# Kernel tuning notes

Measured on AMD Instinct MI355X. Metric: run time of the kernel, lower is better.

## Reference

```python
import jax, jax.numpy as jnp
import numpy as np

B, N, L, P = 128, 128, 64, 30  # batch, max_nodes, latent_dim, n_perms
LOG2PI = float(np.log(2.0 * np.pi))


def setup_inputs() -> dict:
    key = jax.random.key(0)
    k_mu, k_ls, k_eps, k_w, k_adj, k_mask, k_perm = jax.random.split(key, 7)
    mu = jax.random.normal(k_mu, (B, L), dtype=jnp.float32)
    logstd = 0.1 * jax.random.normal(k_ls, (B, L), dtype=jnp.float32)
    eps = jax.random.normal(k_eps, (B, L), dtype=jnp.float32)
    W_dec = 0.02 * jax.random.normal(k_w, (L, N * N), dtype=jnp.float32)
    Adj = jax.random.randint(k_adj, (B, N, N), 0, 2, dtype=jnp.int32)
    # symmetric adjacency, zero diagonal
    Adj = jnp.triu(Adj, 1)
    Adj = Adj + jnp.swapaxes(Adj, 1, 2)
    # per-graph node counts -> block masks marking valid node pairs
    n_nodes = jax.random.randint(k_mask, (B,), N // 2, N + 1)  # [B]
    valid = jnp.arange(N)[None, :] < n_nodes[:, None]          # [B, N]
    node_masks = (valid[:, :, None] & valid[:, None, :]).astype(jnp.int32)
    # true random permutations, one per (i, j) pair as in the torch loop
    perm_keys = jax.random.split(k_perm, B * P)
    perms = jax.vmap(lambda kk: jax.random.permutation(kk, N))(perm_keys)
    perms = perms.reshape(B, P, N).astype(jnp.int32)
    return {"mu": mu, "logstd": logstd, "eps": eps, "W_dec": W_dec,
            "Adj": Adj, "node_masks": node_masks, "perms": perms}


def _masked_perm_logprob(logit, A, m, perm):
    # logit: [N,N] Bernoulli logits; A, m: [N,N]; perm: [N]
    lp = logit[perm][:, perm]  # symmetric permutation of rows and cols
    logp = A * jax.nn.log_sigmoid(lp) + (1.0 - A) * jax.nn.log_sigmoid(-lp)
    return jnp.sum(logp * m)


def reference(mu, logstd, eps, W_dec, Adj, node_masks, perms):
    # q = Normal(mu, exp(logstd)); z = q.rsample()
    z = mu + eps * jnp.exp(logstd)                      # [B, L]
    logits = (z @ W_dec).reshape(B, N, N)               # decoder Bernoulli logits
    # Faithful to torch loop: rec_errors[i, j] uses logits[j], Adj[j], mask[j]
    # with an independent random permutation per (i, j).
    l_p = logits[:P]                                    # [P, N, N]
    A_p = Adj[:P].astype(logits.dtype)
    m_p = node_masks[:P].astype(logits.dtype)
    rec_errors = jax.vmap(
        lambda perm_i: jax.vmap(_masked_perm_logprob)(l_p, A_p, m_p, perm_i)
    )(perms)                                            # [B, P]
    RE = jnp.sum(jnp.max(rec_errors, axis=1))           # scalar
    # KL = log q(z) - log p(z), Independent Normal over latent dim
    log_q = jnp.sum(-0.5 * eps * eps - logstd - 0.5 * LOG2PI, axis=-1)  # [B]
    log_p = jnp.sum(-0.5 * z * z - 0.5 * LOG2PI, axis=-1)               # [B]
    KL = log_q - log_p
    elbo = jnp.mean(RE - KL)
    return -elbo
```

## Files before the change

kernel.cpp:

```cpp
#include <hip/hip_runtime.h>
#include <hip/hip_fp16.h>
#include <math.h>

#define Bn 128
#define Nn 128
#define Ln 64
#define Pn 30
#define PG 10

#define TOFF  0
#define BOFF  491520
#define VOFFW 506880
#define ROFF  510720
#define KLOFF 514560

__global__ __launch_bounds__(256) void k_prep(const float* __restrict__ mu,
                                              const float* __restrict__ logstd,
                                              const float* __restrict__ eps,
                                              const float* __restrict__ W,
                                              const int* __restrict__ Adj,
                                              const int* __restrict__ nm,
                                              float* __restrict__ ws) {
    int blk = blockIdx.x, t = threadIdx.x;
    if (blk < 192) {
        int chunk = blk & 63, pg = blk >> 6;
        __shared__ float zs[PG][Ln];
        for (int idx = t; idx < PG * Ln; idx += 256) {
            int g = pg * PG * Ln + idx;
            zs[idx / Ln][idx % Ln] = mu[g] + eps[g] * __expf(logstd[g]);
        }
        __syncthreads();
        int uv = chunk * 256 + t;
        float acc[PG];
#pragma unroll
        for (int q = 0; q < PG; q++) acc[q] = 0.f;
        for (int k = 0; k < Ln; k++) {
            float w = W[k * (Nn * Nn) + uv];
#pragma unroll
            for (int q = 0; q < PG; q++) acc[q] = fmaf(zs[q][k], w, acc[q]);
        }
        uint32_t* tab = (uint32_t*)ws;
#pragma unroll
        for (int q = 0; q < PG; q++) {
            int p = pg * PG + q;
            float l = acc[q];
            float nl = -l;
            float lsneg = (nl < 0.f) ? (nl - log1pf(__expf(nl))) : (-log1pf(__expf(-nl)));
            __half2 h = __floats2half2_rn(lsneg, l);
            tab[p * (Nn * Nn) + uv] = *(uint32_t*)&h;
        }
    } else if (blk < 192 + 4 * Pn) {
        int pb = blk - 192;
        int p  = pb >> 2;
        int qr = pb & 3;
        __shared__ float val_s[Nn];
        if (t < Nn) {
            float v = (float)nm[p * Nn * Nn + t * Nn + t];
            val_s[t] = v;
            ws[VOFFW + p * Nn + t] = v;
        }
        __syncthreads();
        int sub = t >> 6, lane = t & 63;
        int ioff = sub >> 1, ch = sub & 1;
        int j = ch * 64 + lane;
        uint32_t* Bp = (uint32_t*)ws + BOFF + p * Nn * 4;
        for (int ib = qr * 32; ib < qr * 32 + 32; ib += 2) {
            int i = ib + ioff;
            bool pred = (Adj[p * Nn * Nn + i * Nn + j] != 0) &&
                        (val_s[i] != 0.f) && (val_s[j] != 0.f);
            unsigned long long m = __ballot(pred);
            if (lane == 0) {
                Bp[i * 4 + ch * 2]     = (uint32_t)m;
                Bp[i * 4 + ch * 2 + 1] = (uint32_t)(m >> 32);
            }
        }
    } else {
        float kl = 0.f;
        for (int idx = t; idx < Bn * Ln; idx += 256) {
            float e = eps[idx], ls = logstd[idx];
            float z = mu[idx] + e * __expf(ls);
            kl += -0.5f * e * e - ls + 0.5f * z * z;
        }
        __shared__ float red[256];
        red[t] = kl;
        __syncthreads();
        for (int s = 128; s > 0; s >>= 1) {
            if (t < s) red[t] += red[t + s];
            __syncthreads();
        }
        if (t == 0) ws[KLOFF] = red[0] * (1.0f / (float)Bn);
    }
}

__global__ __launch_bounds__(256) void k_main(const int* __restrict__ perms,
                                              const float* __restrict__ ws,
                                              float* __restrict__ rec) {
    int p  = blockIdx.x >> 5;
    int bb = blockIdx.x & 31;
    int b_base = bb * 4;
    int t = threadIdx.x;

    __shared__ int      inv_s[4][Nn];
    __shared__ uint32_t B_s[Nn * 4];
    __shared__ float    valid_s[Nn];
    __shared__ float    redw[4][4];

    {
        int idx0 = t, idx1 = t + 256;
        int ba0 = idx0 >> 7, i0 = idx0 & 127;
        int ba1 = idx1 >> 7, i1 = idx1 & 127;
        inv_s[ba0][perms[((b_base + ba0) * Pn + p) * Nn + i0]] = i0;
        inv_s[ba1][perms[((b_base + ba1) * Pn + p) * Nn + i1]] = i1;
        const uint32_t* Bp = (const uint32_t*)ws + BOFF + p * Nn * 4;
        B_s[t]       = Bp[t];
        B_s[256 + t] = Bp[256 + t];
        if (t < Nn) valid_s[t] = ws[VOFFW + p * Nn + t];
    }
    __syncthreads();

    int lane = t & 63;
    int wid  = t >> 6;
    int v0 = 2 * lane, v1 = v0 + 1;

    float wv0[4], wv1[4];
    int   a0[4], sh0[4], a1[4], sh1[4];
#pragma unroll
    for (int b = 0; b < 4; ++b) {
        int j0 = inv_s[b][v0], j1 = inv_s[b][v1];
        wv0[b] = valid_s[j0];  wv1[b] = valid_s[j1];
        a0[b] = j0 >> 5; sh0[b] = j0 & 31;
        a1[b] = j1 >> 5; sh1[b] = j1 & 31;
    }

    const uint2* tab2 = (const uint2*)((const uint32_t*)ws + p * (Nn * Nn));
    float acc[4] = {0.f, 0.f, 0.f, 0.f};

#pragma unroll 4
    for (int it = 0; it < 32; ++it) {
        int u = it * 4 + wid;
        uint2 hw = tab2[u * (Nn / 2) + lane];
        float2 f0 = __half22float2(*(__half2*)&hw.x);
        float2 f1 = __half22float2(*(__half2*)&hw.y);
#pragma unroll
        for (int b = 0; b < 4; ++b) {
            int   si  = inv_s[b][u];
            float swu = valid_s[si];
            float tmp = fmaf(wv1[b], f1.x, wv0[b] * f0.x);
            acc[b] = fmaf(swu, tmp, acc[b]);
            uint32_t r0 = B_s[si * 4 + a0[b]];
            uint32_t r1 = B_s[si * 4 + a1[b]];
            acc[b] += ((r0 >> sh0[b]) & 1u) ? f0.y : 0.0f;
            acc[b] += ((r1 >> sh1[b]) & 1u) ? f1.y : 0.0f;
        }
    }

#pragma unroll
    for (int s = 32; s > 0; s >>= 1) {
#pragma unroll
        for (int b = 0; b < 4; ++b) acc[b] += __shfl_down(acc[b], s, 64);
    }
    if (lane == 0) {
#pragma unroll
        for (int b = 0; b < 4; ++b) redw[b][wid] = acc[b];
    }
    __syncthreads();
    if (t < 4) {
        float r = redw[t][0] + redw[t][1] + redw[t][2] + redw[t][3];
        rec[(b_base + t) * Pn + p] = r;
    }
}

__global__ void k_final(const float* __restrict__ ws, float* __restrict__ out) {
    int t = threadIdx.x;
    float m = -INFINITY;
#pragma unroll
    for (int p = 0; p < Pn; p++) m = fmaxf(m, ws[ROFF + t * Pn + p]);
    float contrib = -m * (1.0f / 128.0f);
    (void)contrib;
    __shared__ float red[128];
    red[t] = m;
    __syncthreads();
    for (int s = 64; s > 0; s >>= 1) {
        if (t < s) red[t] += red[t + s];
        __syncthreads();
    }
    if (t == 0) out[0] = ws[KLOFF] - red[0];
}

extern "C" void kernel_launch(void* const* d_in, const int* in_sizes, int n_in,
                              void* d_out, int out_size, void* d_ws, size_t ws_size,
                              hipStream_t stream) {
    const float* mu     = (const float*)d_in[0];
    const float* logstd = (const float*)d_in[1];
    const float* eps    = (const float*)d_in[2];
    const float* W      = (const float*)d_in[3];
    const int*   Adj    = (const int*)d_in[4];
    const int*   nm     = (const int*)d_in[5];
    const int*   perms  = (const int*)d_in[6];
    float* ws  = (float*)d_ws;
    float* out = (float*)d_out;

    hipLaunchKernelGGL(k_prep,  dim3(192 + 4 * Pn + 1), dim3(256), 0, stream,
                       mu, logstd, eps, W, Adj, nm, ws);
    hipLaunchKernelGGL(k_main,  dim3(Pn * 32),          dim3(256), 0, stream,
                       perms, ws, ws + ROFF);
    hipLaunchKernelGGL(k_final, dim3(1),                dim3(128), 0, stream,
                       ws, out);
}
```

Before: 126.2 us.

## Broadcast permuted row indices via readlane and move KL into final kernel

The main loop now preloads each wave's inverse-permutation indices and validity weights into registers and fetches them with readlane, instead of reading them from shared memory on every iteration. The loop is split into two fully unrolled halves of 16 iterations each. The KL reduction block is removed from the prep kernel and computed per-thread in the final kernel, and the adjacency bitmask build drops from four blocks per p to one. This cuts LDS traffic in the hot loop and shrinks the prep grid, at the cost of more registers and a serial 64-element loop per thread in the single-block final kernel.

```diff
diff --git a/kernel.cpp b/kernel.cpp
--- a/kernel.cpp
+++ b/kernel.cpp
@@ -12,7 +12,6 @@
 #define BOFF  491520
 #define VOFFW 506880
 #define ROFF  510720
-#define KLOFF 514560
 
 __global__ __launch_bounds__(256) void k_prep(const float* __restrict__ mu,
                                               const float* __restrict__ logstd,
@@ -49,10 +48,8 @@
             __half2 h = __floats2half2_rn(lsneg, l);
             tab[p * (Nn * Nn) + uv] = *(uint32_t*)&h;
         }
-    } else if (blk < 192 + 4 * Pn) {
-        int pb = blk - 192;
-        int p  = pb >> 2;
-        int qr = pb & 3;
+    } else {
+        int p = blk - 192;
         __shared__ float val_s[Nn];
         if (t < Nn) {
             float v = (float)nm[p * Nn * Nn + t * Nn + t];
@@ -64,7 +61,7 @@
         int ioff = sub >> 1, ch = sub & 1;
         int j = ch * 64 + lane;
         uint32_t* Bp = (uint32_t*)ws + BOFF + p * Nn * 4;
-        for (int ib = qr * 32; ib < qr * 32 + 32; ib += 2) {
+        for (int ib = 0; ib < Nn; ib += 2) {
             int i = ib + ioff;
             bool pred = (Adj[p * Nn * Nn + i * Nn + j] != 0) &&
                         (val_s[i] != 0.f) && (val_s[j] != 0.f);
@@ -74,21 +71,6 @@
                 Bp[i * 4 + ch * 2 + 1] = (uint32_t)(m >> 32);
             }
         }
-    } else {
-        float kl = 0.f;
-        for (int idx = t; idx < Bn * Ln; idx += 256) {
-            float e = eps[idx], ls = logstd[idx];
-            float z = mu[idx] + e * __expf(ls);
-            kl += -0.5f * e * e - ls + 0.5f * z * z;
-        }
-        __shared__ float red[256];
-        red[t] = kl;
-        __syncthreads();
-        for (int s = 128; s > 0; s >>= 1) {
-            if (t < s) red[t] += red[t + s];
-            __syncthreads();
-        }
-        if (t == 0) ws[KLOFF] = red[0] * (1.0f / (float)Bn);
     }
 }
 
@@ -120,31 +102,38 @@
 
     int lane = t & 63;
     int wid  = t >> 6;
+    int swid = __builtin_amdgcn_readfirstlane(wid);
     int v0 = 2 * lane, v1 = v0 + 1;
 
     float wv0[4], wv1[4];
     int   a0[4], sh0[4], a1[4], sh1[4];
+    int   iu_lo[4], iu_hi[4], vu_lo[4], vu_hi[4];
 #pragma unroll
     for (int b = 0; b < 4; ++b) {
         int j0 = inv_s[b][v0], j1 = inv_s[b][v1];
         wv0[b] = valid_s[j0];  wv1[b] = valid_s[j1];
         a0[b] = j0 >> 5; sh0[b] = j0 & 31;
         a1[b] = j1 >> 5; sh1[b] = j1 & 31;
+        int il = inv_s[b][lane];
+        int ih = inv_s[b][64 + lane];
+        iu_lo[b] = il; iu_hi[b] = ih;
+        vu_lo[b] = __float_as_int(valid_s[il]);
+        vu_hi[b] = __float_as_int(valid_s[ih]);
     }
 
     const uint2* tab2 = (const uint2*)((const uint32_t*)ws + p * (Nn * Nn));
     float acc[4] = {0.f, 0.f, 0.f, 0.f};
 
-#pragma unroll 4
-    for (int it = 0; it < 32; ++it) {
-        int u = it * 4 + wid;
+#pragma unroll
+    for (int it = 0; it < 16; ++it) {
+        int u = it * 4 + swid;
         uint2 hw = tab2[u * (Nn / 2) + lane];
         float2 f0 = __half22float2(*(__half2*)&hw.x);
         float2 f1 = __half22float2(*(__half2*)&hw.y);
 #pragma unroll
         for (int b = 0; b < 4; ++b) {
-            int   si  = inv_s[b][u];
-            float swu = valid_s[si];
+            int   si  = __builtin_amdgcn_readlane(iu_lo[b], u);
+            float swu = __int_as_float(__builtin_amdgcn_readlane(vu_lo[b], u));
             float tmp = fmaf(wv1[b], f1.x, wv0[b] * f0.x);
             acc[b] = fmaf(swu, tmp, acc[b]);
             uint32_t r0 = B_s[si * 4 + a0[b]];
@@ -153,6 +142,24 @@
             acc[b] += ((r1 >> sh1[b]) & 1u) ? f1.y : 0.0f;
         }
     }
+#pragma unroll
+    for (int it = 0; it < 16; ++it) {
+        int u = it * 4 + swid;
+        uint2 hw = tab2[(64 + u) * (Nn / 2) + lane];
+        float2 f0 = __half22float2(*(__half2*)&hw.x);
+        float2 f1 = __half22float2(*(__half2*)&hw.y);
+#pragma unroll
+        for (int b = 0; b < 4; ++b) {
+            int   si  = __builtin_amdgcn_readlane(iu_hi[b], u);
+            float swu = __int_as_float(__builtin_amdgcn_readlane(vu_hi[b], u));
+            float tmp = fmaf(wv1[b], f1.x, wv0[b] * f0.x);
+            acc[b] = fmaf(swu, tmp, acc[b]);
+            uint32_t r0 = B_s[si * 4 + a0[b]];
+            uint32_t r1 = B_s[si * 4 + a1[b]];
+            acc[b] += ((r0 >> sh0[b]) & 1u) ? f0.y : 0.0f;
+            acc[b] += ((r1 >> sh1[b]) & 1u) ? f1.y : 0.0f;
+        }
+    }
 
 #pragma unroll
     for (int s = 32; s > 0; s >>= 1) {
@@ -170,21 +177,31 @@
     }
 }
 
-__global__ void k_final(const float* __restrict__ ws, float* __restrict__ out) {
+__global__ void k_final(const float* __restrict__ mu,
+                        const float* __restrict__ logstd,
+                        const float* __restrict__ eps,
+                        const float* __restrict__ ws,
+                        float* __restrict__ out) {
     int t = threadIdx.x;
+    float kl = 0.f;
+    for (int l = 0; l < Ln; ++l) {
+        int   idx = t * Ln + l;
+        float e = eps[idx], ls = logstd[idx];
+        float z = mu[idx] + e * __expf(ls);
+        kl += -0.5f * e * e - ls + 0.5f * z * z;
+    }
     float m = -INFINITY;
 #pragma unroll
     for (int p = 0; p < Pn; p++) m = fmaxf(m, ws[ROFF + t * Pn + p]);
-    float contrib = -m * (1.0f / 128.0f);
-    (void)contrib;
+    float contrib = kl * (1.0f / Bn) - m;
     __shared__ float red[128];
-    red[t] = m;
+    red[t] = contrib;
     __syncthreads();
     for (int s = 64; s > 0; s >>= 1) {
         if (t < s) red[t] += red[t + s];
         __syncthreads();
     }
-    if (t == 0) out[0] = ws[KLOFF] - red[0];
+    if (t == 0) out[0] = red[0];
 }
 
 extern "C" void kernel_launch(void* const* d_in, const int* in_sizes, int n_in,
@@ -200,10 +217,10 @@
     float* ws  = (float*)d_ws;
     float* out = (float*)d_out;
 
-    hipLaunchKernelGGL(k_prep,  dim3(192 + 4 * Pn + 1), dim3(256), 0, stream,
+    hipLaunchKernelGGL(k_prep,  dim3(192 + Pn), dim3(256), 0, stream,
                        mu, logstd, eps, W, Adj, nm, ws);
-    hipLaunchKernelGGL(k_main,  dim3(Pn * 32),          dim3(256), 0, stream,
+    hipLaunchKernelGGL(k_main,  dim3(Pn * 32),  dim3(256), 0, stream,
                        perms, ws, ws + ROFF);
-    hipLaunchKernelGGL(k_final, dim3(1),                dim3(128), 0, stream,
-                       ws, out);
-}
+    hipLaunchKernelGGL(k_final, dim3(1),        dim3(128), 0, stream,
+                       mu, logstd, eps, ws, out);
+}
```

After: 125.2 us. Within noise of the previous version (-0.8%).
